# Kernel tuning notes

Measured on AMD Instinct MI355X. Metric: run time of the kernel, lower is better.

## Reference

```python
import jax, jax.numpy as jnp
import numpy as np

B, N, T, D = 32, 19, 2048, 128
TOP_K = 3
THRESHOLD = 1e-4
TEMPERATURE = 0.1


def setup_inputs() -> dict:
    key = jax.random.key(0)
    features = jax.random.normal(key, (B, N, T, D), dtype=jnp.float32)
    return {"features": features}


def reference(features):
    b, n, t, d = features.shape
    # (B, N, T, D) -> (B*T, N, D)
    f = features.transpose(0, 2, 1, 3).reshape(b * t, n, d)
    # cosine similarity (F.normalize uses eps=1e-12 on the norm)
    norm = jnp.linalg.norm(f, axis=-1, keepdims=True)
    fn = f / jnp.maximum(norm, 1e-12)
    adj = jnp.einsum('bnd,bmd->bnm', fn, fn) / TEMPERATURE
    adj = jax.nn.softmax(adj, axis=-1)
    # top-k sparsification along last dim
    vals, idx = jax.lax.top_k(adj, TOP_K)
    adj = jnp.put_along_axis(jnp.zeros_like(adj), idx, vals, axis=-1, inplace=False)
    # threshold pruning
    adj = jnp.where(adj > THRESHOLD, adj, jnp.zeros_like(adj))
    # symmetrize
    adj = (adj + adj.transpose(0, 2, 1)) * 0.5
    return adj.reshape(b, t, n, n)
```

## Files before the change

kernel.cpp:

```cpp
#include <hip/hip_runtime.h>
#include <math.h>

namespace {

constexpr int kB = 32;
constexpr int kN = 19;
constexpr int kT = 2048;
constexpr int kD = 128;

constexpr int TILES = 32;
constexpr int TPT   = 10;
constexpr int BDIM  = TILES * TPT;
constexpr int RPAD  = 21;
constexpr int TSTR  = 400;

constexpr float kTempInv = 10.0f;
constexpr float kThresh  = 1e-4f;

__global__ __launch_bounds__(BDIM, 2)
void fused_graph_kernel(const float* __restrict__ feat, float* __restrict__ out)
{
    __shared__ float sG[TILES * TSTR];
    __shared__ float sInv[TILES * 20];

    const int tid = threadIdx.x;
    const int tl  = tid / TPT;
    const int sub = tid - tl * TPT;
    const int bi    = (sub >= 4) + (sub >= 7) + (sub >= 9);
    const int start = bi * 4 - (bi * (bi - 1)) / 2;
    const int bj    = bi + (sub - start);

    const int gt0 = blockIdx.x * TILES;
    const int b0  = gt0 >> 11;
    const int t0  = gt0 & (kT - 1);
    const float* tb = feat + ((size_t)b0 * kN * kT + (size_t)(t0 + tl)) * kD;

    const float* pa[5];
    const float* pb[5];
#pragma unroll
    for (int r = 0; r < 5; ++r) {
        int ar = bi * 5 + r; if (ar > kN - 1) ar = kN - 1;
        pa[r] = tb + (size_t)ar * (kT * kD);
    }
#pragma unroll
    for (int c = 0; c < 5; ++c) {
        int bc = bj * 5 + c; if (bc > kN - 1) bc = kN - 1;
        pb[c] = tb + (size_t)bc * (kT * kD);
    }

    float acc[5][5];
#pragma unroll
    for (int r = 0; r < 5; ++r)
#pragma unroll
        for (int c = 0; c < 5; ++c) acc[r][c] = 0.f;

    for (int k = 0; k < kD; k += 4) {
        float4 ra[5], cb[5];
#pragma unroll
        for (int r = 0; r < 5; ++r)
            ra[r] = *(const float4*)(pa[r] + k);
        if (bi == bj) {
#pragma unroll
            for (int c = 0; c < 5; ++c) cb[c] = ra[c];
        } else {
#pragma unroll
            for (int c = 0; c < 5; ++c)
                cb[c] = *(const float4*)(pb[c] + k);
        }
#pragma unroll
        for (int r = 0; r < 5; ++r)
#pragma unroll
            for (int c = 0; c < 5; ++c) {
                acc[r][c] = fmaf(ra[r].x, cb[c].x, acc[r][c]);
                acc[r][c] = fmaf(ra[r].y, cb[c].y, acc[r][c]);
                acc[r][c] = fmaf(ra[r].z, cb[c].z, acc[r][c]);
                acc[r][c] = fmaf(ra[r].w, cb[c].w, acc[r][c]);
            }
    }

    {
        float* g = &sG[tl * TSTR];
#pragma unroll
        for (int r = 0; r < 5; ++r) {
            const int i = bi * 5 + r;
#pragma unroll
            for (int c = 0; c < 5; ++c) {
                const int j = bj * 5 + c;
                if (i < kN && j < kN) {
                    g[i * RPAD + j] = acc[r][c];
                    if (i != j) g[j * RPAD + i] = acc[r][c];
                }
            }
        }
    }
    __syncthreads();

    for (int q = tid; q < TILES * kN; q += BDIM) {
        const int tt = q / kN;
        const int i  = q - tt * kN;
        const float nrm = sqrtf(sG[tt * TSTR + i * RPAD + i]);
        sInv[tt * 20 + i] = 1.0f / fmaxf(nrm, 1e-12f);
    }
    __syncthreads();

    for (int q = tid; q < TILES * kN; q += BDIM) {
        const int tt = q / kN;
        const int i  = q - tt * kN;
        float* row = &sG[tt * TSTR + i * RPAD];
        const float* invp = &sInv[tt * 20];
        const float si = invp[i] * kTempInv;

        float l[kN];
        float m = -3.0e38f;
#pragma unroll
        for (int j = 0; j < kN; ++j) {
            const float g = row[j] * si * invp[j];
            l[j] = g;
            m = fmaxf(m, g);
        }
        float ssum = 0.f;
#pragma unroll
        for (int j = 0; j < kN; ++j) {
            const float e = __expf(l[j] - m);
            l[j] = e;
            ssum += e;
        }
        const float rs = 1.0f / ssum;
#pragma unroll
        for (int j = 0; j < kN; ++j) l[j] *= rs;

        int k1 = 0; float v1 = -1.f;
#pragma unroll
        for (int j = 0; j < kN; ++j) if (l[j] > v1) { v1 = l[j]; k1 = j; }
        int k2 = -1; float v2 = -1.f;
#pragma unroll
        for (int j = 0; j < kN; ++j) if (j != k1 && l[j] > v2) { v2 = l[j]; k2 = j; }
        int k3 = -1; float v3 = -1.f;
#pragma unroll
        for (int j = 0; j < kN; ++j) if (j != k1 && j != k2 && l[j] > v3) { v3 = l[j]; k3 = j; }

#pragma unroll
        for (int j = 0; j < kN; ++j) {
            const float p = l[j];
            const bool keep = (j == k1 || j == k2 || j == k3) && (p > kThresh);
            row[j] = keep ? p : 0.f;
        }
    }
    __syncthreads();

    float* ob = out + (size_t)gt0 * (kN * kN);
    for (int q = tid; q < TILES * kN * kN; q += BDIM) {
        const int tt = q / (kN * kN);
        const int r  = q - tt * (kN * kN);
        const int i  = r / kN;
        const int j  = r - i * kN;
        const float v = 0.5f * (sG[tt * TSTR + i * RPAD + j] +
                                sG[tt * TSTR + j * RPAD + i]);
        ob[q] = v;
    }
}

}

extern "C" void kernel_launch(void* const* d_in, const int* in_sizes, int n_in,
                              void* d_out, int out_size, void* d_ws, size_t ws_size,
                              hipStream_t stream)
{
    const float* feat = (const float*)d_in[0];
    float* out = (float*)d_out;
    dim3 grid((kB * kT) / TILES);
    dim3 block(BDIM);
    hipLaunchKernelGGL(fused_graph_kernel, grid, block, 0, stream, feat, out);
}
```

Before: 1.160 ms.

## Stage feature chunks cooperatively in shared memory before Gram accumulation

Instead of each thread loading its own row blocks straight from global memory, the block now cooperatively copies 16-wide D chunks of all 19 nodes for its 32 time steps into shared memory with coalesced float4 loads. The Gram tile is then computed from LDS, with a rotated sub-chunk index to spread bank accesses. This removes the redundant global reads made by threads that share rows and gives better coalescing. The cost is two barriers per chunk with no double buffering, and the shared buffer is reused later for the Gram matrix.

```diff
diff --git a/kernel.cpp b/kernel.cpp
--- a/kernel.cpp
+++ b/kernel.cpp
@@ -11,6 +11,10 @@
 constexpr int TILES = 32;
 constexpr int TPT   = 10;
 constexpr int BDIM  = TILES * TPT;
+constexpr int KC    = 16;
+constexpr int SROW  = kN * KC;
+constexpr int CHUNK_F4 = TILES * kN * (KC / 4);
+
 constexpr int RPAD  = 21;
 constexpr int TSTR  = 400;
 
@@ -20,7 +24,7 @@
 __global__ __launch_bounds__(BDIM, 2)
 void fused_graph_kernel(const float* __restrict__ feat, float* __restrict__ out)
 {
-    __shared__ float sG[TILES * TSTR];
+    __shared__ float smem[TILES * TSTR];
     __shared__ float sInv[TILES * 20];
 
     const int tid = threadIdx.x;
@@ -33,20 +37,14 @@
     const int gt0 = blockIdx.x * TILES;
     const int b0  = gt0 >> 11;
     const int t0  = gt0 & (kT - 1);
-    const float* tb = feat + ((size_t)b0 * kN * kT + (size_t)(t0 + tl)) * kD;
 
-    const float* pa[5];
-    const float* pb[5];
+    const float* blkBase = feat + ((size_t)b0 * kN * kT + (size_t)t0) * kD;
+
+    int ar[5], bc[5];
 #pragma unroll
-    for (int r = 0; r < 5; ++r) {
-        int ar = bi * 5 + r; if (ar > kN - 1) ar = kN - 1;
-        pa[r] = tb + (size_t)ar * (kT * kD);
-    }
+    for (int r = 0; r < 5; ++r) { ar[r] = bi * 5 + r; if (ar[r] > kN - 1) ar[r] = kN - 1; }
 #pragma unroll
-    for (int c = 0; c < 5; ++c) {
-        int bc = bj * 5 + c; if (bc > kN - 1) bc = kN - 1;
-        pb[c] = tb + (size_t)bc * (kT * kD);
-    }
+    for (int c = 0; c < 5; ++c) { bc[c] = bj * 5 + c; if (bc[c] > kN - 1) bc[c] = kN - 1; }
 
     float acc[5][5];
 #pragma unroll
@@ -54,32 +52,47 @@
 #pragma unroll
         for (int c = 0; c < 5; ++c) acc[r][c] = 0.f;
 
-    for (int k = 0; k < kD; k += 4) {
-        float4 ra[5], cb[5];
+    for (int kc = 0; kc < kD; kc += KC) {
+        for (int q = tid; q < CHUNK_F4; q += BDIM) {
+            const int d4 = q & 3;
+            const int t  = (q >> 2) & (TILES - 1);
+            const int n  = q >> 7;
+            const float4 v = *(const float4*)(blkBase + ((size_t)n << 18) + ((size_t)t << 7) + kc + d4 * 4);
+            *(float4*)(&smem[t * SROW + n * KC + d4 * 4]) = v;
+        }
+        __syncthreads();
+
+        const float* base = &smem[tl * SROW];
 #pragma unroll
-        for (int r = 0; r < 5; ++r)
-            ra[r] = *(const float4*)(pa[r] + k);
-        if (bi == bj) {
+        for (int s0 = 0; s0 < 4; ++s0) {
+            const int s = (s0 + sub) & 3;
+            float4 ra[5], cb[5];
 #pragma unroll
-            for (int c = 0; c < 5; ++c) cb[c] = ra[c];
-        } else {
+            for (int r = 0; r < 5; ++r)
+                ra[r] = *(const float4*)(base + ar[r] * KC + s * 4);
+            if (bi == bj) {
 #pragma unroll
-            for (int c = 0; c < 5; ++c)
-                cb[c] = *(const float4*)(pb[c] + k);
+                for (int c = 0; c < 5; ++c) cb[c] = ra[c];
+            } else {
+#pragma unroll
+                for (int c = 0; c < 5; ++c)
+                    cb[c] = *(const float4*)(base + bc[c] * KC + s * 4);
+            }
+#pragma unroll
+            for (int r = 0; r < 5; ++r)
+#pragma unroll
+                for (int c = 0; c < 5; ++c) {
+                    acc[r][c] = fmaf(ra[r].x, cb[c].x, acc[r][c]);
+                    acc[r][c] = fmaf(ra[r].y, cb[c].y, acc[r][c]);
+                    acc[r][c] = fmaf(ra[r].z, cb[c].z, acc[r][c]);
+                    acc[r][c] = fmaf(ra[r].w, cb[c].w, acc[r][c]);
+                }
         }
-#pragma unroll
-        for (int r = 0; r < 5; ++r)
-#pragma unroll
-            for (int c = 0; c < 5; ++c) {
-                acc[r][c] = fmaf(ra[r].x, cb[c].x, acc[r][c]);
-                acc[r][c] = fmaf(ra[r].y, cb[c].y, acc[r][c]);
-                acc[r][c] = fmaf(ra[r].z, cb[c].z, acc[r][c]);
-                acc[r][c] = fmaf(ra[r].w, cb[c].w, acc[r][c]);
-            }
+        __syncthreads();
     }
 
     {
-        float* g = &sG[tl * TSTR];
+        float* g = &smem[tl * TSTR];
 #pragma unroll
         for (int r = 0; r < 5; ++r) {
             const int i = bi * 5 + r;
@@ -98,7 +111,7 @@
     for (int q = tid; q < TILES * kN; q += BDIM) {
         const int tt = q / kN;
         const int i  = q - tt * kN;
-        const float nrm = sqrtf(sG[tt * TSTR + i * RPAD + i]);
+        const float nrm = sqrtf(smem[tt * TSTR + i * RPAD + i]);
         sInv[tt * 20 + i] = 1.0f / fmaxf(nrm, 1e-12f);
     }
     __syncthreads();
@@ -106,7 +119,7 @@
     for (int q = tid; q < TILES * kN; q += BDIM) {
         const int tt = q / kN;
         const int i  = q - tt * kN;
-        float* row = &sG[tt * TSTR + i * RPAD];
+        float* row = &smem[tt * TSTR + i * RPAD];
         const float* invp = &sInv[tt * 20];
         const float si = invp[i] * kTempInv;
 
@@ -154,8 +167,8 @@
         const int r  = q - tt * (kN * kN);
         const int i  = r / kN;
         const int j  = r - i * kN;
-        const float v = 0.5f * (sG[tt * TSTR + i * RPAD + j] +
-                                sG[tt * TSTR + j * RPAD + i]);
+        const float v = 0.5f * (smem[tt * TSTR + i * RPAD + j] +
+                                smem[tt * TSTR + j * RPAD + i]);
         ob[q] = v;
     }
 }
```

After: 1.062 ms. 8.5% less time.
